# Kernel optimization log

Measured on AMD Instinct MI355X. Metric: run time of the kernel, lower is better.

Reference implementation:

```python
import jax, jax.numpy as jnp
import numpy as np

B, N, IN_F, OUT_F, H = 4, 2048, 256, 256, 8
NH = OUT_F // H  # 32
SLOPE = 0.2
NEG_INF = -9e15


def setup_inputs() -> dict:
    key = jax.random.key(0)
    k1, k2, k3, k4 = jax.random.split(key, 4)
    h = jax.random.normal(k1, (B, N, IN_F), jnp.float32)
    adj = jax.random.randint(k2, (B, N, N), 0, 2).astype(jnp.int32)
    # xavier_uniform with gain 1.414
    gw = 1.414 * np.sqrt(6.0 / (IN_F + H * NH))
    W = jax.random.uniform(k3, (IN_F, H * NH), jnp.float32, -gw, gw)
    ga = 1.414 * np.sqrt(6.0 / (2 * NH + 1))
    a = jax.random.uniform(k4, (2 * NH, 1), jnp.float32, -ga, ga)
    return {"h": h, "adj": adj, "W": W, "a": a}


def reference(h, adj, W, a):
    Wh = h @ W                              # [B, N, H*NH]
    # Faithful to torch .view: raw memory reinterpretation, not a transpose.
    Wh = Wh.reshape(B, H, N, NH)            # [B, H, N, NH]
    Wh1 = Wh @ a[:NH]                       # [B, H, N, 1]
    Wh2 = Wh @ a[NH:]                       # [B, H, N, 1]
    e = Wh1 + jnp.swapaxes(Wh2, 2, 3)       # [B, H, N, N] additive scores
    e = jnp.where(e >= 0, e, SLOPE * e)     # leaky relu
    e = jnp.where(adj[:, None] > 0, e, NEG_INF)
    attn = jax.nn.softmax(e, axis=-1)       # [B, H, N, N]
    h_prime = attn @ Wh                     # [B, H, N, NH]
    h_prime = h_prime.reshape(B, N, OUT_F)  # raw reshape, matches torch .view
    return jax.nn.elu(h_prime)
```

## Files before the change

kernel.cpp:

```cpp
#include <hip/hip_runtime.h>
#include <hip/hip_bf16.h>

#define B_    4
#define N_    2048
#define INF_  256
#define OUTF_ 256
#define H_    8
#define NH_   32
#define BH_   (B_ * H_)
#define ROWS_ (B_ * N_)
#define VSZ_  (N_ * NH_)

typedef float  f32x4 __attribute__((ext_vector_type(4)));
typedef short  s16x8 __attribute__((ext_vector_type(8)));

static __device__ __forceinline__ short f2bf(float x) {
    union { __hip_bfloat16 b; unsigned short u; } cv;
    cv.b = __float2bfloat16(x);
    return (short)cv.u;
}

__global__ __launch_bounds__(256) void prep(const int* __restrict__ adj,
                                            unsigned int* __restrict__ adjw,
                                            const float* __restrict__ h,
                                            const float* __restrict__ W,
                                            short* __restrict__ hb,
                                            short* __restrict__ Wf) {
    const int blk = blockIdx.x;
    const int tid = threadIdx.x;
    if (blk < 2048) {
        const int idx = blk * 256 + tid;
        const int4* p = (const int4*)(adj + (size_t)idx * 32);
        unsigned int w = 0;
#pragma unroll
        for (int q = 0; q < 8; ++q) {
            int4 v = p[q];
            w |= (v.x != 0 ? 1u : 0u) << (q * 4 + 0);
            w |= (v.y != 0 ? 1u : 0u) << (q * 4 + 1);
            w |= (v.z != 0 ? 1u : 0u) << (q * 4 + 2);
            w |= (v.w != 0 ? 1u : 0u) << (q * 4 + 3);
        }
        adjw[idx] = w;
    } else if (blk < 3072) {
        const int t = (blk - 2048) * 256 + tid;
        const float4* src = (const float4*)(h + (size_t)t * 8);
        float4 v0 = src[0], v1 = src[1];
        float vv[8] = {v0.x, v0.y, v0.z, v0.w, v1.x, v1.y, v1.z, v1.w};
        s16x8 o;
#pragma unroll
        for (int i = 0; i < 8; ++i) o[i] = f2bf(vv[i]);
        *(s16x8*)(hb + (size_t)t * 8) = o;
    } else {
        const int u = (blk - 3072) * 256 + tid;
        const int lane = u & 63, nf = (u >> 6) & 15, kt = u >> 10;
        const float* src = W + (size_t)(kt * 32 + (lane >> 4) * 8) * 256 +
                           nf * 16 + (lane & 15);
        s16x8 o;
#pragma unroll
        for (int i = 0; i < 8; ++i) o[i] = f2bf(src[(size_t)i * 256]);
        *(s16x8*)(Wf + (size_t)u * 8) = o;
    }
}

__global__ __launch_bounds__(256) void gemm_stv(const short* __restrict__ hb,
                                                const short* __restrict__ Wf,
                                                const float* __restrict__ a,
                                                float* __restrict__ rS,
                                                float2* __restrict__ tE,
                                                short* __restrict__ Vb) {
    const int bm  = blockIdx.x * 64;
    const int bn4 = blockIdx.y * 4;
    const int tid = threadIdx.x;
    const int wv = tid >> 6, l = tid & 63;
    const int lr = l & 15, lg = l >> 4;
    const int arow = bm + wv * 16 + lr;

    f32x4 acc[4] = {};
    const s16x8* wf = (const s16x8*)Wf;
    const s16x8* ha = (const s16x8*)(hb + (size_t)arow * 256 + lg * 8);

#pragma unroll
    for (int kt = 0; kt < 8; ++kt) {
        s16x8 av = ha[kt * 4];
#pragma unroll
        for (int nf = 0; nf < 4; ++nf) {
            s16x8 b = wf[(size_t)(kt * 16 + bn4 + nf) * 64 + l];
            acc[nf] = __builtin_amdgcn_mfma_f32_16x16x32_bf16(av, b, acc[nf], 0, 0, 0);
        }
    }

    {
        const int bh  = bm >> 8;
        const int rr0 = (bm & 255) + wv * 16 + 4 * lg;
        short* vout = Vb + (size_t)bh * 65536;
#pragma unroll
        for (int nf = 0; nf < 4; ++nf) {
            const int nt = nf & 1;
            const int ch = (bn4 + nf) >> 1;
#pragma unroll
            for (int r = 0; r < 4; ++r) {
                const int rr = rr0 + r;
                vout[((rr >> 2) * 2 + nt) * 512 + ((rr & 3) * 16 + lr) * 8 + ch] =
                    f2bf(acc[nf][r]);
            }
        }
    }

    const float a1lo = a[lr],      a1hi = a[16 + lr];
    const float a2lo = a[32 + lr], a2hi = a[48 + lr];
#pragma unroll
    for (int k = 0; k < 2; ++k) {
#pragma unroll
        for (int r = 0; r < 4; ++r) {
            float ps = acc[2 * k][r] * a1lo + acc[2 * k + 1][r] * a1hi;
            float pt = acc[2 * k][r] * a2lo + acc[2 * k + 1][r] * a2hi;
#pragma unroll
            for (int d = 1; d < 16; d <<= 1) {
                ps += __shfl_xor(ps, d);
                pt += __shfl_xor(pt, d);
            }
            if (lr == 0) {
                const int R  = bm + wv * 16 + 4 * lg + r;
                const int b  = R >> 11, rin = R & 2047;
                const int hh = rin >> 8, rr = rin & 255;
                const int n  = rr * 8 + (bn4 >> 1) + k;
                const int g  = ((b * 8 + hh) << 11) + n;
                rS[g] = __expf(-0.8f * ps);
                tE[g] = make_float2(__expf(pt), __expf(0.2f * pt));
            }
        }
    }
}

__global__ __launch_bounds__(256, 4) void attn_kernel(const short* __restrict__ Vb,
                                                      const float* __restrict__ rS,
                                                      const float2* __restrict__ tE,
                                                      const unsigned int* __restrict__ adjw,
                                                      float* __restrict__ out) {
    const int bh = blockIdx.y;
    const int b  = bh >> 3;
    const int i0 = blockIdx.x * 64;
    const int tid = threadIdx.x;
    const int wv = tid >> 6;
    const int l  = tid & 63;
    const int lr = l & 15;
    const int lg = l >> 4;

    __shared__ int    adjL[64][68];
    __shared__ float4 ts4[1024];

    {
        const int4* ab = (const int4*)(adjw + (size_t)(b * N_ + i0) * 64);
#pragma unroll
        for (int k = 0; k < 4; ++k) {
            int idx4 = tid + k * 256;
            int4 v = ab[idx4];
            *(int4*)&adjL[idx4 >> 4][(idx4 << 2) & 63] = v;
        }
    }
    {
        const float4* tsrc = (const float4*)(tE + (size_t)bh * N_);
#pragma unroll
        for (int k = 0; k < 4; ++k) ts4[tid + k * 256] = tsrc[tid + k * 256];
    }
    const float rr_i = rS[(size_t)bh * N_ + i0 + wv * 16 + lr];
    __syncthreads();

    s16x8 bOnes;
#pragma unroll
    for (int i = 0; i < 8; ++i) bOnes[i] = (lr == 0) ? (short)0x3F80 : (short)0;

    const s16x8* vb = (const s16x8*)(Vb + (size_t)bh * 65536);
    const int*    adjRow = &adjL[wv * 16 + lr][0];
    const float4* tsRow  = ts4 + lg * 4;

    f32x4 acc0 = {0.f, 0.f, 0.f, 0.f};
    f32x4 acc1 = {0.f, 0.f, 0.f, 0.f};
    f32x4 acc2 = {0.f, 0.f, 0.f, 0.f};

    auto tile = [&](int jtc, const s16x8& B0, const s16x8& B1) {
        const unsigned wsh = ((unsigned)adjRow[jtc]) >> (lg * 8);
        const float4* qp = tsRow + jtc * 16;
        float4 q0 = qp[0];
        float4 q1 = qp[1];
        float4 q2 = qp[2];
        float4 q3 = qp[3];
        float p[8];
        p[0] = fmaxf(q0.x, rr_i * q0.y);
        p[1] = fmaxf(q0.z, rr_i * q0.w);
        p[2] = fmaxf(q1.x, rr_i * q1.y);
        p[3] = fmaxf(q1.z, rr_i * q1.w);
        p[4] = fmaxf(q2.x, rr_i * q2.y);
        p[5] = fmaxf(q2.z, rr_i * q2.w);
        p[6] = fmaxf(q3.x, rr_i * q3.y);
        p[7] = fmaxf(q3.z, rr_i * q3.w);
        unsigned pu[8];
#pragma unroll
        for (int i = 0; i < 8; ++i) {
            const int m = ((int)(wsh << (31 - i))) >> 31;
            pu[i] = __float_as_uint(p[i]) & (unsigned)m;
        }
        union { unsigned u[4]; s16x8 v; } af;
#pragma unroll
        for (int q = 0; q < 4; ++q)
            asm("v_cvt_pk_bf16_f32 %0, %1, %2"
                : "=v"(af.u[q])
                : "v"(__uint_as_float(pu[2 * q])), "v"(__uint_as_float(pu[2 * q + 1])));
        acc0 = __builtin_amdgcn_mfma_f32_16x16x32_bf16(af.v, B0, acc0, 0, 0, 0);
        acc1 = __builtin_amdgcn_mfma_f32_16x16x32_bf16(af.v, B1, acc1, 0, 0, 0);
        acc2 = __builtin_amdgcn_mfma_f32_16x16x32_bf16(af.v, bOnes, acc2, 0, 0, 0);
    };

    s16x8 cb0 = vb[l], cb1 = vb[64 + l];
    for (int jt0 = 0; jt0 < 56; jt0 += 8) {
#pragma unroll
        for (int k = 0; k < 8; ++k) {
            const int jt = jt0 + k;
            s16x8 nb0 = vb[(jt + 1) * 128 + l];
            s16x8 nb1 = vb[(jt + 1) * 128 + 64 + l];
            tile(jt, cb0, cb1);
            cb0 = nb0; cb1 = nb1;
        }
    }
#pragma unroll
    for (int k = 0; k < 8; ++k) {
        const int jt = 56 + k;
        if (k < 7) {
            s16x8 nb0 = vb[(jt + 1) * 128 + l];
            s16x8 nb1 = vb[(jt + 1) * 128 + 64 + l];
            tile(jt, cb0, cb1);
            cb0 = nb0; cb1 = nb1;
        } else {
            tile(jt, cb0, cb1);
        }
    }

    float* obase = out + (size_t)bh * VSZ_;
#pragma unroll
    for (int r = 0; r < 4; ++r) {
        const int rloc = 4 * lg + r;
        const float rsum = __shfl(acc2[r], (l & 48));
        const float ir = 1.0f / rsum;
        const int row = i0 + wv * 16 + rloc;
        float v0 = acc0[r] * ir;
        float v1 = acc1[r] * ir;
        v0 = v0 > 0.f ? v0 : expm1f(v0);
        v1 = v1 > 0.f ? v1 : expm1f(v1);
        obase[(size_t)row * NH_ + lr]      = v0;
        obase[(size_t)row * NH_ + 16 + lr] = v1;
    }
}

extern "C" void kernel_launch(void* const* d_in, const int* in_sizes, int n_in,
                              void* d_out, int out_size, void* d_ws, size_t ws_size,
                              hipStream_t stream) {
    const float* h   = (const float*)d_in[0];
    const int*   adj = (const int*)d_in[1];
    const float* W   = (const float*)d_in[2];
    const float* a   = (const float*)d_in[3];
    float* out = (float*)d_out;

    char* ws = (char*)d_ws;
    float*  rS = (float*)ws;
    float2* tE = (float2*)(ws + (size_t)BH_ * N_ * 8);
    unsigned int* adjw = (unsigned int*)(ws + 2 * (size_t)BH_ * N_ * 8);
    char* p2 = ws + 2 * (size_t)BH_ * N_ * 8 + (size_t)B_ * N_ * 64 * 4;
    short* Vb = (short*)p2;
    short* hb = (short*)(p2 + (size_t)BH_ * VSZ_ * 2);
    short* Wf = (short*)(p2 + (size_t)BH_ * VSZ_ * 2 + (size_t)ROWS_ * INF_ * 2);

    prep<<<3104, 256, 0, stream>>>(adj, adjw, h, W, hb, Wf);
    gemm_stv<<<dim3(ROWS_ / 64, OUTF_ / 64), 256, 0, stream>>>(hb, Wf, a, rS, tE, Vb);
    attn_kernel<<<dim3(N_ / 64, BH_), 256, 0, stream>>>(Vb, rS, tE, adjw, out);
}
```

Baseline: 146.4 us.

## Split attention over key dimension into two partial blocks with merge kernel

The attention kernel is split along the key (j) dimension into two halves via a third grid dimension, doubling the block count. Each half writes unnormalized numerators and denominators to workspace buffers, and a new merge kernel sums them, normalizes and applies ELU. The aim is better occupancy and latency hiding across CUs, at the cost of an extra launch and extra global traffic for the partial results. The launch-bounds occupancy hint is also dropped.

```diff
diff --git a/kernel.cpp b/kernel.cpp
--- a/kernel.cpp
+++ b/kernel.cpp
@@ -132,36 +132,38 @@
     }
 }
 
-__global__ __launch_bounds__(256, 4) void attn_kernel(const short* __restrict__ Vb,
-                                                      const float* __restrict__ rS,
-                                                      const float2* __restrict__ tE,
-                                                      const unsigned int* __restrict__ adjw,
-                                                      float* __restrict__ out) {
+__global__ __launch_bounds__(256) void attn_part(const short* __restrict__ Vb,
+                                                 const float* __restrict__ rS,
+                                                 const float2* __restrict__ tE,
+                                                 const unsigned int* __restrict__ adjw,
+                                                 float* __restrict__ pnum,
+                                                 float* __restrict__ pden) {
     const int bh = blockIdx.y;
     const int b  = bh >> 3;
     const int i0 = blockIdx.x * 64;
+    const int jz = blockIdx.z;
     const int tid = threadIdx.x;
     const int wv = tid >> 6;
     const int l  = tid & 63;
     const int lr = l & 15;
     const int lg = l >> 4;
 
-    __shared__ int    adjL[64][68];
-    __shared__ float4 ts4[1024];
+    __shared__ int    adjL[64][36];
+    __shared__ float4 ts4[512];
 
     {
-        const int4* ab = (const int4*)(adjw + (size_t)(b * N_ + i0) * 64);
-#pragma unroll
-        for (int k = 0; k < 4; ++k) {
-            int idx4 = tid + k * 256;
-            int4 v = ab[idx4];
-            *(int4*)&adjL[idx4 >> 4][(idx4 << 2) & 63] = v;
+        const int4* ab4 = (const int4*)(adjw + ((size_t)(b * N_ + i0)) * 64 + jz * 32);
+#pragma unroll
+        for (int k = 0; k < 2; ++k) {
+            const int idx4 = tid + k * 256;
+            int4 v = ab4[(idx4 >> 3) * 16 + (idx4 & 7)];
+            *(int4*)&adjL[idx4 >> 3][(idx4 & 7) << 2] = v;
         }
     }
     {
-        const float4* tsrc = (const float4*)(tE + (size_t)bh * N_);
-#pragma unroll
-        for (int k = 0; k < 4; ++k) ts4[tid + k * 256] = tsrc[tid + k * 256];
+        const float4* tsrc = (const float4*)(tE + (size_t)bh * N_) + jz * 512;
+        ts4[tid]       = tsrc[tid];
+        ts4[tid + 256] = tsrc[tid + 256];
     }
     const float rr_i = rS[(size_t)bh * N_ + i0 + wv * 16 + lr];
     __syncthreads();
@@ -170,7 +172,7 @@
 #pragma unroll
     for (int i = 0; i < 8; ++i) bOnes[i] = (lr == 0) ? (short)0x3F80 : (short)0;
 
-    const s16x8* vb = (const s16x8*)(Vb + (size_t)bh * 65536);
+    const s16x8* vbz = (const s16x8*)(Vb + (size_t)bh * 65536) + (size_t)jz * 32 * 128;
     const int*    adjRow = &adjL[wv * 16 + lr][0];
     const float4* tsRow  = ts4 + lg * 4;
 
@@ -211,23 +213,23 @@
         acc2 = __builtin_amdgcn_mfma_f32_16x16x32_bf16(af.v, bOnes, acc2, 0, 0, 0);
     };
 
-    s16x8 cb0 = vb[l], cb1 = vb[64 + l];
-    for (int jt0 = 0; jt0 < 56; jt0 += 8) {
+    s16x8 cb0 = vbz[l], cb1 = vbz[64 + l];
+    for (int jt0 = 0; jt0 < 24; jt0 += 8) {
 #pragma unroll
         for (int k = 0; k < 8; ++k) {
             const int jt = jt0 + k;
-            s16x8 nb0 = vb[(jt + 1) * 128 + l];
-            s16x8 nb1 = vb[(jt + 1) * 128 + 64 + l];
+            s16x8 nb0 = vbz[(jt + 1) * 128 + l];
+            s16x8 nb1 = vbz[(jt + 1) * 128 + 64 + l];
             tile(jt, cb0, cb1);
             cb0 = nb0; cb1 = nb1;
         }
     }
 #pragma unroll
     for (int k = 0; k < 8; ++k) {
-        const int jt = 56 + k;
+        const int jt = 24 + k;
         if (k < 7) {
-            s16x8 nb0 = vb[(jt + 1) * 128 + l];
-            s16x8 nb1 = vb[(jt + 1) * 128 + 64 + l];
+            s16x8 nb0 = vbz[(jt + 1) * 128 + l];
+            s16x8 nb1 = vbz[(jt + 1) * 128 + 64 + l];
             tile(jt, cb0, cb1);
             cb0 = nb0; cb1 = nb1;
         } else {
@@ -235,20 +237,38 @@
         }
     }
 
-    float* obase = out + (size_t)bh * VSZ_;
+    float* pn = pnum + ((size_t)jz * BH_ * N_ + (size_t)bh * N_) * 32;
+    float* pd = pden + (size_t)jz * BH_ * N_ + (size_t)bh * N_;
 #pragma unroll
     for (int r = 0; r < 4; ++r) {
         const int rloc = 4 * lg + r;
-        const float rsum = __shfl(acc2[r], (l & 48));
-        const float ir = 1.0f / rsum;
-        const int row = i0 + wv * 16 + rloc;
-        float v0 = acc0[r] * ir;
-        float v1 = acc1[r] * ir;
-        v0 = v0 > 0.f ? v0 : expm1f(v0);
-        v1 = v1 > 0.f ? v1 : expm1f(v1);
-        obase[(size_t)row * NH_ + lr]      = v0;
-        obase[(size_t)row * NH_ + 16 + lr] = v1;
-    }
+        const int row = i0 + rloc + wv * 16;
+        pn[(size_t)row * 32 + lr]      = acc0[r];
+        pn[(size_t)row * 32 + 16 + lr] = acc1[r];
+        if (lr == 0) pd[row] = acc2[r];
+    }
+}
+
+__global__ __launch_bounds__(256) void merge(const float* __restrict__ pnum,
+                                             const float* __restrict__ pden,
+                                             float* __restrict__ out) {
+    const int t = blockIdx.x * 256 + threadIdx.x;
+    const int row = t >> 2;
+    const int c8 = (t & 3) * 8;
+    const float* n0 = pnum + (size_t)row * 32 + c8;
+    const float* n1 = pnum + (size_t)BH_ * N_ * 32 + (size_t)row * 32 + c8;
+    const float ir = 1.0f / (pden[row] + pden[BH_ * N_ + row]);
+    float4 a0 = *(const float4*)n0, a1 = *(const float4*)(n0 + 4);
+    float4 b0 = *(const float4*)n1, b1 = *(const float4*)(n1 + 4);
+    float o[8] = {a0.x + b0.x, a0.y + b0.y, a0.z + b0.z, a0.w + b0.w,
+                  a1.x + b1.x, a1.y + b1.y, a1.z + b1.z, a1.w + b1.w};
+#pragma unroll
+    for (int i = 0; i < 8; ++i) {
+        float v = o[i] * ir;
+        o[i] = v > 0.f ? v : expm1f(v);
+    }
+    *(float4*)(out + (size_t)row * 32 + c8)     = *(float4*)&o[0];
+    *(float4*)(out + (size_t)row * 32 + c8 + 4) = *(float4*)&o[4];
 }
 
 extern "C" void kernel_launch(void* const* d_in, const int* in_sizes, int n_in,
@@ -268,8 +288,12 @@
     short* Vb = (short*)p2;
     short* hb = (short*)(p2 + (size_t)BH_ * VSZ_ * 2);
     short* Wf = (short*)(p2 + (size_t)BH_ * VSZ_ * 2 + (size_t)ROWS_ * INF_ * 2);
+    char* p3 = p2 + (size_t)BH_ * VSZ_ * 2 + (size_t)ROWS_ * INF_ * 2 + 8192 * 16;
+    float* pnum = (float*)p3;
+    float* pden = (float*)(p3 + 2 * (size_t)BH_ * N_ * 32 * 4);
 
     prep<<<3104, 256, 0, stream>>>(adj, adjw, h, W, hb, Wf);
     gemm_stv<<<dim3(ROWS_ / 64, OUTF_ / 64), 256, 0, stream>>>(hb, Wf, a, rS, tE, Vb);
-    attn_kernel<<<dim3(N_ / 64, BH_), 256, 0, stream>>>(Vb, rS, tE, adjw, out);
-}
+    attn_part<<<dim3(N_ / 64, BH_, 2), 256, 0, stream>>>(Vb, rS, tE, adjw, pnum, pden);
+    merge<<<1024, 256, 0, stream>>>(pnum, pden, out);
+}
```

Result: slower. 150.8 us (+3.0%).
